# Optimization experiments

Hardware: AMD Instinct MI355X
Metric: run time of the kernel (lower is better)

Reference implementation:

```python
import jax, jax.numpy as jnp
import numpy as np

TOP_K = 2
LB_WEIGHT = 0.01


def _ln(x, g, b, eps=1e-5):
    m = x.mean(-1, keepdims=True)
    v = ((x - m) ** 2).mean(-1, keepdims=True)
    return (x - m) * jax.lax.rsqrt(v + eps) * g + b


def setup_inputs() -> dict:
    key = jax.random.key(0)
    ks = iter(jax.random.split(key, 40))
    B, L, D, CT, CB, E, H = 8, 1024, 1024, 768, 64, 8, 1024
    ID = 3 * D           # concat(id, content_proj, collab_proj)
    GH = max(ID // 2, 128)  # 1536, router gate hidden

    def rn(shape, s=0.02):
        return jax.random.normal(next(ks), shape, jnp.float32) * s

    return {
        "id_emb": rn((B, L, D), 1.0),
        "content_emb": rn((B, L, CT), 1.0),
        "collab_emb": rn((B, L, CB), 1.0),
        "ln_ct_g": jnp.ones(CT), "ln_ct_b": jnp.zeros(CT),
        "ln_cb_g": jnp.ones(CB), "ln_cb_b": jnp.zeros(CB),
        "Wc": rn((CT, D)), "bc": jnp.zeros(D),
        "Wcb": rn((CB, D)), "bcb": jnp.zeros(D),
        "Wg1": rn((ID, GH)), "bg1": jnp.zeros(GH),
        "lng_g": jnp.ones(GH), "lng_b": jnp.zeros(GH),
        "Wg2": rn((GH, GH // 2)), "bg2": jnp.zeros(GH // 2),
        "Wg3": rn((GH // 2, E)), "bg3": jnp.zeros(E),
        "We1": rn((E, ID, H)), "be1": jnp.zeros((E, H)),
        "lne1_g": jnp.ones((E, H)), "lne1_b": jnp.zeros((E, H)),
        "We2": rn((E, H, H // 2)), "be2": jnp.zeros((E, H // 2)),
        "We3": rn((E, H // 2, H // 4)), "be3": jnp.zeros((E, H // 4)),
        "lne3_g": jnp.ones((E, H // 4)), "lne3_b": jnp.zeros((E, H // 4)),
        "Wout": rn((H // 4, D)), "bout": jnp.zeros(D),
        "alpha": jnp.full((1,), 0.1, jnp.float32),
    }


def reference(id_emb, content_emb, collab_emb, ln_ct_g, ln_ct_b, ln_cb_g, ln_cb_b,
              Wc, bc, Wcb, bcb, Wg1, bg1, lng_g, lng_b, Wg2, bg2, Wg3, bg3,
              We1, be1, lne1_g, lne1_b, We2, be2, We3, be3, lne3_g, lne3_b,
              Wout, bout, alpha):
    # --- input normalization + projection to d_model (eval mode: no noise/dropout) ---
    ct = _ln(content_emb, ln_ct_g, ln_ct_b) @ Wc + bc        # (B,L,D)
    cb = _ln(collab_emb, ln_cb_g, ln_cb_b) @ Wcb + bcb       # (B,L,D)
    x = jnp.concatenate([id_emb, ct, cb], axis=-1)           # (B,L,3D)

    # --- router: gate MLP -> softmax -> top-k -> renormalize ---
    g = jax.nn.relu(_ln(x @ Wg1 + bg1, lng_g, lng_b))
    g = jax.nn.relu(g @ Wg2 + bg2)
    probs = jax.nn.softmax(g @ Wg3 + bg3, axis=-1)           # (B,L,E)
    topv, topi = jax.lax.top_k(probs, TOP_K)                 # (B,L,K)
    w = topv / (topv.sum(-1, keepdims=True) + 1e-8)

    # --- experts (dense over E, then gather selected) ---
    h = jax.nn.relu(_ln(jnp.einsum('bld,edh->bleh', x, We1) + be1, lne1_g, lne1_b))
    h = jax.nn.relu(jnp.einsum('bleh,ehm->blem', h, We2) + be2)
    eo = _ln(jnp.einsum('blem,emo->bleo', h, We3) + be3, lne3_g, lne3_b)  # (B,L,E,H/4)
    sel = jnp.take_along_axis(eo, topi[..., None], axis=2)   # (B,L,K,H/4)
    comb = (sel * w[..., None]).sum(axis=2)                  # (B,L,H/4)

    # --- output projection + learnable-alpha residual ---
    fused = id_emb + alpha * (comb @ Wout + bout)            # (B,L,D)

    # --- load balancing loss (importance + entropy terms) ---
    E = probs.shape[-1]
    num_tokens = probs.shape[0] * probs.shape[1]
    counts = jnp.sum(jax.nn.one_hot(topi, E, dtype=jnp.float32), axis=(0, 1, 2))
    f = counts / num_tokens
    P = probs.mean(axis=(0, 1))
    importance = E * (f * P).sum()
    ent = -(P * jnp.log(P + 1e-8)).sum()
    max_ent = jnp.log(jnp.asarray(E, jnp.float32))
    lb_loss = (importance + (max_ent - ent) / max_ent) * LB_WEIGHT
    return fused, lb_loss
```

## Files before the change

### kernel.cpp

```cpp
#include <hip/hip_runtime.h>
#include <hip/hip_bf16.h>

using u16 = unsigned short;
typedef float f32x4 __attribute__((ext_vector_type(4)));
typedef short short8 __attribute__((ext_vector_type(8)));
typedef unsigned short ushort8 __attribute__((ext_vector_type(8)));

typedef __attribute__((address_space(1))) const unsigned int gu32;
typedef __attribute__((address_space(3))) unsigned int lu32;

__device__ __forceinline__ float b2f(u16 u) {
  unsigned v = ((unsigned)u) << 16;
  float f;
  __builtin_memcpy(&f, &v, 4);
  return f;
}
__device__ __forceinline__ u16 f2b(float f) {
  unsigned u;
  __builtin_memcpy(&u, &f, 4);
  unsigned r = (u + 0x7fffu + ((u >> 16) & 1u)) >> 16;
  return (u16)r;
}
__device__ __forceinline__ float ldv(float x) { return x; }
__device__ __forceinline__ float ldv(u16 x) { return b2f(x); }

__device__ __forceinline__ void gl_lds16(const void* g, void* l) {
  __builtin_amdgcn_global_load_lds((gu32*)g, (lu32*)l, 16, 0, 0);
}

template <int D, bool RELU, bool PEREXP, typename TIN>
__global__ void ln_rows(const TIN* __restrict__ in, u16* __restrict__ out,
                        const float* __restrict__ gamma, const float* __restrict__ beta,
                        const int* __restrict__ pairExp, const int* __restrict__ total) {
  constexpr int T = (D >= 256) ? 256 : 64;
  constexpr int VPT = D / T;
  int row = blockIdx.x;
  if constexpr (PEREXP) {
    if (row >= *total) return;
  }
  int t = threadIdx.x;
  const TIN* r = in + (size_t)row * D;
  float vals[VPT];
  float s = 0.f, ss = 0.f;
#pragma unroll
  for (int i = 0; i < VPT; ++i) {
    float v = ldv(r[t + i * T]);
    vals[i] = v;
    s += v;
    ss += v * v;
  }
#pragma unroll
  for (int m = 1; m < 64; m <<= 1) {
    s += __shfl_xor(s, m);
    ss += __shfl_xor(ss, m);
  }
  if constexpr (T == 256) {
    __shared__ float red[8];
    int wave = t >> 6, lane = t & 63;
    if (lane == 0) { red[wave] = s; red[4 + wave] = ss; }
    __syncthreads();
    s = red[0] + red[1] + red[2] + red[3];
    ss = red[4] + red[5] + red[6] + red[7];
  }
  float mean = s / (float)D;
  float var = ss / (float)D - mean * mean;
  var = fmaxf(var, 0.f);
  float rstd = 1.f / sqrtf(var + 1e-5f);
  const float* g = gamma;
  const float* b = beta;
  if constexpr (PEREXP) {
    int e = pairExp[row];
    g += (size_t)e * D;
    b += (size_t)e * D;
  }
  u16* o = out + (size_t)row * D;
#pragma unroll
  for (int i = 0; i < VPT; ++i) {
    int idx = t + i * T;
    float v = (vals[i] - mean) * rstd * g[idx] + b[idx];
    if constexpr (RELU) v = fmaxf(v, 0.f);
    o[idx] = f2b(v);
  }
}

__global__ void prepackT(const float* __restrict__ in, u16* __restrict__ out,
                         int K, int M) {
  __shared__ u16 tile[64 * 65];
  size_t zo = (size_t)blockIdx.z * K * M;
  const float* ip = in + zo;
  u16* op = out + zo;
  int m0 = blockIdx.x * 64, k0 = blockIdx.y * 64;
  int t = threadIdx.x;
#pragma unroll
  for (int h = 0; h < 4; ++h) {
    int u = t + h * 256;
    int kr = u >> 4, mc = (u & 15) * 4;
    f32x4 v = *(const f32x4*)(ip + (size_t)(k0 + kr) * M + m0 + mc);
#pragma unroll
    for (int i = 0; i < 4; ++i) tile[kr * 65 + mc + i] = f2b(v[i]);
  }
  __syncthreads();
#pragma unroll
  for (int h = 0; h < 2; ++h) {
    int u = t + h * 256;
    int mr = u >> 3, kc = (u & 7) * 8;
    ushort8 v;
#pragma unroll
    for (int i = 0; i < 8; ++i) v[i] = tile[(kc + i) * 65 + mr];
    *(ushort8*)(op + (size_t)(m0 + mr) * K + k0 + kc) = v;
  }
}

__global__ void copy_id3(const float* __restrict__ id, u16* __restrict__ xb3) {
  size_t i = ((size_t)blockIdx.x * 256 + threadIdx.x) * 8;
  size_t t = i >> 10, d = i & 1023;
  f32x4 a = *(const f32x4*)(id + i);
  f32x4 b = *(const f32x4*)(id + i + 4);
  ushort8 v;
#pragma unroll
  for (int j = 0; j < 4; ++j) { v[j] = f2b(a[j]); v[j + 4] = f2b(b[j]); }
  *(ushort8*)(xb3 + t * 3072 + d) = v;
}

#define BM 128
#define BN 128
#define BK 32

template <int EPI, bool EXPERT, bool GATHER>
__global__ __launch_bounds__(256, 4)
void gemm_bf(const u16* __restrict__ A, const u16* __restrict__ Bt,
             const float* __restrict__ bias,
             u16* __restrict__ C, float* __restrict__ Cf,
             int K, int lda, int ldc,
             long strideB, int strideBias,
             const int* __restrict__ offA, const int* __restrict__ pairTok,
             const float* __restrict__ resid, const float* __restrict__ alphaPtr) {
  int rowTile = blockIdx.x * BM;
  int colTile = blockIdx.y * BN;
  if constexpr (EXPERT) {
    if (rowTile >= offA[8]) return;
    int e = 0;
    while (rowTile >= offA[e + 1]) ++e;
    Bt += (size_t)e * strideB;
    bias += (size_t)e * strideBias;
  }

  __shared__ u16 As[2][BM * BK];
  __shared__ u16 Bs[2][BN * BK];

  int t = threadIdx.x;
  int lane = t & 63;
  int wv = t >> 6;
  int wr = wv >> 1, wc = wv & 1;
  int l15 = lane & 15, l4 = lane >> 4;

  int c0 = wv, c1 = wv + 4;
  int r0 = c0 * 16 + (lane >> 2), r1 = c1 * 16 + (lane >> 2);
  int ac = (lane & 3) * 8;
  size_t aRow0, aRow1;
  if constexpr (GATHER) {
    aRow0 = (size_t)pairTok[rowTile + r0] * lda;
    aRow1 = (size_t)pairTok[rowTile + r1] * lda;
  } else {
    aRow0 = (size_t)(rowTile + r0) * lda;
    aRow1 = (size_t)(rowTile + r1) * lda;
  }
  const u16* aSrc0 = A + aRow0 + ac;
  const u16* aSrc1 = A + aRow1 + ac;
  const u16* bSrc0 = Bt + (size_t)(colTile + r0) * K + ac;
  const u16* bSrc1 = Bt + (size_t)(colTile + r1) * K + ac;

  auto STAGE = [&](int k0, int b) {
    gl_lds16(aSrc0 + k0, &As[b][c0 * 512]);
    gl_lds16(aSrc1 + k0, &As[b][c1 * 512]);
    gl_lds16(bSrc0 + k0, &Bs[b][c0 * 512]);
    gl_lds16(bSrc1 + k0, &Bs[b][c1 * 512]);
  };

  f32x4 zero4 = {0.f, 0.f, 0.f, 0.f};
  f32x4 acc[4][4];
#pragma unroll
  for (int m = 0; m < 4; ++m)
#pragma unroll
    for (int n = 0; n < 4; ++n) acc[m][n] = zero4;

  STAGE(0, 0);
  asm volatile("s_waitcnt vmcnt(0)" ::: "memory");
  __syncthreads();

  int nt = K / BK;
  for (int tt = 0; tt < nt; ++tt) {
    int cur = tt & 1;
    if (tt + 1 < nt) STAGE((tt + 1) * BK, cur ^ 1);
    short8 af[4], bf[4];
#pragma unroll
    for (int m = 0; m < 4; ++m)
      af[m] = *(const short8*)&As[cur][(wr * 64 + m * 16 + l15) * BK + l4 * 8];
#pragma unroll
    for (int n = 0; n < 4; ++n)
      bf[n] = *(const short8*)&Bs[cur][(wc * 64 + n * 16 + l15) * BK + l4 * 8];
#pragma unroll
    for (int m = 0; m < 4; ++m)
#pragma unroll
      for (int n = 0; n < 4; ++n)
        acc[m][n] = __builtin_amdgcn_mfma_f32_16x16x32_bf16(af[m], bf[n], acc[m][n], 0, 0, 0);
    asm volatile("s_waitcnt vmcnt(0)" ::: "memory");
    __syncthreads();
  }

  float alphaV = 0.f;
  if constexpr (EPI == 2) alphaV = alphaPtr[0];
#pragma unroll
  for (int n = 0; n < 4; ++n) {
    int col = colTile + wc * 64 + n * 16 + l15;
    float bv = bias[col];
#pragma unroll
    for (int m = 0; m < 4; ++m) {
      int r2 = rowTile + wr * 64 + m * 16 + l4 * 4;
#pragma unroll
      for (int j = 0; j < 4; ++j) {
        float v = acc[m][n][j] + bv;
        if constexpr (EPI == 1) v = fmaxf(v, 0.f);
        if constexpr (EPI == 2) {
          Cf[(size_t)(r2 + j) * ldc + col] =
              resid[(size_t)(r2 + j) * ldc + col] + alphaV * v;
        } else {
          C[(size_t)(r2 + j) * ldc + col] = f2b(v);
        }
      }
    }
  }
}

__global__ void router_kernel(const u16* __restrict__ g2, const float* __restrict__ Wg3,
                              const float* __restrict__ bg3, float* __restrict__ probs,
                              int* __restrict__ topi, float* __restrict__ wts) {
  int tok = blockIdx.x * 4 + (threadIdx.x >> 6);
  int lane = threadIdx.x & 63;
  const u16* row = g2 + (size_t)tok * 768;
  float acc[8];
#pragma unroll
  for (int e = 0; e < 8; ++e) acc[e] = 0.f;
  for (int j = lane; j < 768; j += 64) {
    float v = b2f(row[j]);
    f32x4 w0 = *(const f32x4*)(Wg3 + (size_t)j * 8);
    f32x4 w1 = *(const f32x4*)(Wg3 + (size_t)j * 8 + 4);
#pragma unroll
    for (int e = 0; e < 4; ++e) { acc[e] += v * w0[e]; acc[e + 4] += v * w1[e]; }
  }
#pragma unroll
  for (int e = 0; e < 8; ++e) {
#pragma unroll
    for (int m = 1; m < 64; m <<= 1) acc[e] += __shfl_xor(acc[e], m);
  }
  if (lane == 0) {
    float lg[8], mx = -3.4e38f;
#pragma unroll
    for (int e = 0; e < 8; ++e) {
      lg[e] = acc[e] + bg3[e];
      mx = fmaxf(mx, lg[e]);
    }
    float p[8], s = 0.f;
#pragma unroll
    for (int e = 0; e < 8; ++e) {
      p[e] = expf(lg[e] - mx);
      s += p[e];
    }
    float inv = 1.f / s;
#pragma unroll
    for (int e = 0; e < 8; ++e) {
      p[e] *= inv;
      probs[(size_t)tok * 8 + e] = p[e];
    }
    int i0 = 0;
    for (int e = 1; e < 8; ++e)
      if (p[e] > p[i0]) i0 = e;
    int i1 = (i0 == 0) ? 1 : 0;
    for (int e = 0; e < 8; ++e)
      if (e != i0 && p[e] > p[i1]) i1 = e;
    float w0 = p[i0], w1 = p[i1];
    float wsum = w0 + w1 + 1e-8f;
    topi[tok * 2] = i0;
    topi[tok * 2 + 1] = i1;
    wts[tok * 2] = w0 / wsum;
    wts[tok * 2 + 1] = w1 / wsum;
  }
}

__global__ void count_kernel(const int* __restrict__ topi, int* __restrict__ cnt,
                             int* __restrict__ offA, int* __restrict__ cursor) {
  __shared__ int c[8];
  int t = threadIdx.x;
  if (t < 8) c[t] = 0;
  __syncthreads();
  for (int i = t; i < 16384; i += 256) atomicAdd(&c[topi[i]], 1);
  __syncthreads();
  if (t == 0) {
    int off = 0;
    for (int e = 0; e < 8; ++e) {
      cnt[e] = c[e];
      offA[e] = off;
      cursor[e] = off;
      off += (c[e] + 127) & ~127;
    }
    offA[8] = off;
  }
}

__global__ void scatter_kernel(const int* __restrict__ topi, int* __restrict__ cursor,
                               int* __restrict__ pairTok, int* __restrict__ pairExp,
                               int* __restrict__ posOf) {
  int i = blockIdx.x * 256 + threadIdx.x;
  int e = topi[i];
  int pos = atomicAdd(&cursor[e], 1);
  pairTok[pos] = i >> 1;
  pairExp[pos] = e;
  posOf[i] = pos;
}

__global__ void padfill_kernel(const int* __restrict__ cnt, const int* __restrict__ offA,
                               int* __restrict__ pairTok, int* __restrict__ pairExp) {
  int e = blockIdx.x;
  int start = offA[e] + cnt[e];
  int end = offA[e + 1];
  for (int i = start + threadIdx.x; i < end; i += 256) {
    pairTok[i] = 0;
    pairExp[i] = e;
  }
}

__global__ void combine_kernel(const u16* __restrict__ eo, const int* __restrict__ posOf,
                               const float* __restrict__ wts, u16* __restrict__ comb) {
  int t = blockIdx.x, d = threadIdx.x;
  int p0 = posOf[t * 2], p1 = posOf[t * 2 + 1];
  float w0 = wts[t * 2], w1 = wts[t * 2 + 1];
  float v = w0 * b2f(eo[(size_t)p0 * 256 + d]) + w1 * b2f(eo[(size_t)p1 * 256 + d]);
  comb[(size_t)t * 256 + d] = f2b(v);
}

__global__ void lbloss_kernel(const float* __restrict__ probs, const int* __restrict__ cnt,
                              float* __restrict__ outp) {
  __shared__ float red[256];
  int t = threadIdx.x;
  float pl[8];
#pragma unroll
  for (int e = 0; e < 8; ++e) pl[e] = 0.f;
  for (int i = t; i < 8192; i += 256) {
#pragma unroll
    for (int e = 0; e < 8; ++e) pl[e] += probs[(size_t)i * 8 + e];
  }
  float P[8];
  for (int e = 0; e < 8; ++e) {
    red[t] = pl[e];
    __syncthreads();
    for (int s = 128; s > 0; s >>= 1) {
      if (t < s) red[t] += red[t + s];
      __syncthreads();
    }
    P[e] = red[0] / 8192.f;
    __syncthreads();
  }
  if (t == 0) {
    float imp = 0.f, ent = 0.f;
    for (int e = 0; e < 8; ++e) {
      float f = (float)cnt[e] / 8192.f;
      imp += f * P[e];
      ent -= P[e] * logf(P[e] + 1e-8f);
    }
    imp *= 8.f;
    float maxent = logf(8.f);
    outp[0] = (imp + (maxent - ent) / maxent) * 0.01f;
  }
}

extern "C" void kernel_launch(void* const* d_in, const int* in_sizes, int n_in,
                              void* d_out, int out_size, void* d_ws, size_t ws_size,
                              hipStream_t stream) {
  const float* id_emb   = (const float*)d_in[0];
  const float* content  = (const float*)d_in[1];
  const float* collab   = (const float*)d_in[2];
  const float* ln_ct_g  = (const float*)d_in[3];
  const float* ln_ct_b  = (const float*)d_in[4];
  const float* ln_cb_g  = (const float*)d_in[5];
  const float* ln_cb_b  = (const float*)d_in[6];
  const float* Wc       = (const float*)d_in[7];
  const float* bc       = (const float*)d_in[8];
  const float* Wcb      = (const float*)d_in[9];
  const float* bcb      = (const float*)d_in[10];
  const float* Wg1      = (const float*)d_in[11];
  const float* bg1      = (const float*)d_in[12];
  const float* lng_g    = (const float*)d_in[13];
  const float* lng_b    = (const float*)d_in[14];
  const float* Wg2      = (const float*)d_in[15];
  const float* bg2      = (const float*)d_in[16];
  const float* Wg3      = (const float*)d_in[17];
  const float* bg3      = (const float*)d_in[18];
  const float* We1      = (const float*)d_in[19];
  const float* be1      = (const float*)d_in[20];
  const float* lne1_g   = (const float*)d_in[21];
  const float* lne1_b   = (const float*)d_in[22];
  const float* We2      = (const float*)d_in[23];
  const float* be2      = (const float*)d_in[24];
  const float* We3      = (const float*)d_in[25];
  const float* be3      = (const float*)d_in[26];
  const float* lne3_g   = (const float*)d_in[27];
  const float* lne3_b   = (const float*)d_in[28];
  const float* Wout     = (const float*)d_in[29];
  const float* bout     = (const float*)d_in[30];
  const float* alpha    = (const float*)d_in[31];
  (void)in_sizes; (void)n_in; (void)out_size; (void)ws_size;

  float* out = (float*)d_out;
  char* ws = (char*)d_ws;
  size_t o = 0;
  auto AL = [&](size_t bytes) {
    size_t r = o;
    o += (bytes + 255) & ~(size_t)255;
    return r;
  };

  u16* WcT   = (u16*)(ws + AL(1024ull * 768 * 2));
  u16* WcbT  = (u16*)(ws + AL(1024ull * 64 * 2));
  u16* Wg1T  = (u16*)(ws + AL(1536ull * 3072 * 2));
  u16* Wg2T  = (u16*)(ws + AL(768ull * 1536 * 2));
  u16* We1T  = (u16*)(ws + AL(8ull * 1024 * 3072 * 2));
  u16* We2T  = (u16*)(ws + AL(8ull * 512 * 1024 * 2));
  u16* We3T  = (u16*)(ws + AL(8ull * 256 * 512 * 2));
  u16* WoutT = (u16*)(ws + AL(1024ull * 256 * 2));
  u16* xb3   = (u16*)(ws + AL(8192ull * 3072 * 2));
  size_t R1  = AL(17408ull * 1024 * 2);
  u16* ct_norm = (u16*)(ws + R1);
  u16* cb_norm = (u16*)(ws + R1 + 8192ull * 768 * 2);
  u16* g1      = (u16*)(ws + R1);
  u16* h1      = (u16*)(ws + R1);
  size_t R2  = AL(17408ull * 512 * 2);
  u16* g2 = (u16*)(ws + R2);
  u16* h2 = (u16*)(ws + R2);
  u16* eo   = (u16*)(ws + AL(17408ull * 256 * 2));
  u16* comb = (u16*)(ws + AL(8192ull * 256 * 2));
  float* probs = (float*)(ws + AL(8192ull * 8 * 4));
  int* topi    = (int*)(ws + AL(8192ull * 2 * 4));
  float* wts   = (float*)(ws + AL(8192ull * 2 * 4));
  int* posOf   = (int*)(ws + AL(8192ull * 2 * 4));
  int* pairTok = (int*)(ws + AL(17408ull * 4));
  int* pairExp = (int*)(ws + AL(17408ull * 4));
  int* cnt     = (int*)(ws + AL(64));
  int* offA    = (int*)(ws + AL(64));
  int* cursor  = (int*)(ws + AL(64));

  prepackT<<<dim3(16, 12), 256, 0, stream>>>(Wc, WcT, 768, 1024);
  prepackT<<<dim3(16, 1), 256, 0, stream>>>(Wcb, WcbT, 64, 1024);
  prepackT<<<dim3(24, 48), 256, 0, stream>>>(Wg1, Wg1T, 3072, 1536);
  prepackT<<<dim3(12, 24), 256, 0, stream>>>(Wg2, Wg2T, 1536, 768);
  prepackT<<<dim3(16, 48, 8), 256, 0, stream>>>(We1, We1T, 3072, 1024);
  prepackT<<<dim3(8, 16, 8), 256, 0, stream>>>(We2, We2T, 1024, 512);
  prepackT<<<dim3(4, 8, 8), 256, 0, stream>>>(We3, We3T, 512, 256);
  prepackT<<<dim3(16, 4), 256, 0, stream>>>(Wout, WoutT, 256, 1024);

  ln_rows<768, false, false, float><<<8192, 256, 0, stream>>>(content, ct_norm, ln_ct_g, ln_ct_b, nullptr, nullptr);
  ln_rows<64, false, false, float><<<8192, 64, 0, stream>>>(collab, cb_norm, ln_cb_g, ln_cb_b, nullptr, nullptr);
  copy_id3<<<4096, 256, 0, stream>>>(id_emb, xb3);
  gemm_bf<0, false, false><<<dim3(64, 8), 256, 0, stream>>>(
      ct_norm, WcT, bc, xb3 + 1024, nullptr, 768, 768, 3072,
      0, 0, nullptr, nullptr, nullptr, nullptr);
  gemm_bf<0, false, false><<<dim3(64, 8), 256, 0, stream>>>(
      cb_norm, WcbT, bcb, xb3 + 2048, nullptr, 64, 64, 3072,
      0, 0, nullptr, nullptr, nullptr, nullptr);

  gemm_bf<0, false, false><<<dim3(64, 12), 256, 0, stream>>>(
      xb3, Wg1T, bg1, g1, nullptr, 3072, 3072, 1536,
      0, 0, nullptr, nullptr, nullptr, nullptr);
  ln_rows<1536, true, false, u16><<<8192, 256, 0, stream>>>(g1, g1, lng_g, lng_b, nullptr, nullptr);
  gemm_bf<1, false, false><<<dim3(64, 6), 256, 0, stream>>>(
      g1, Wg2T, bg2, g2, nullptr, 1536, 1536, 768,
      0, 0, nullptr, nullptr, nullptr, nullptr);
  router_kernel<<<2048, 256, 0, stream>>>(g2, Wg3, bg3, probs, topi, wts);

  count_kernel<<<1, 256, 0, stream>>>(topi, cnt, offA, cursor);
  scatter_kernel<<<64, 256, 0, stream>>>(topi, cursor, pairTok, pairExp, posOf);
  padfill_kernel<<<8, 256, 0, stream>>>(cnt, offA, pairTok, pairExp);

  gemm_bf<0, true, true><<<dim3(136, 8), 256, 0, stream>>>(
      xb3, We1T, be1, h1, nullptr, 3072, 3072, 1024,
      3072l * 1024, 1024, offA, pairTok, nullptr, nullptr);
  ln_rows<1024, true, true, u16><<<17408, 256, 0, stream>>>(h1, h1, lne1_g, lne1_b, pairExp, offA + 8);
  gemm_bf<1, true, false><<<dim3(136, 4), 256, 0, stream>>>(
      h1, We2T, be2, h2, nullptr, 1024, 1024, 512,
      512l * 1024, 512, offA, nullptr, nullptr, nullptr);
  gemm_bf<0, true, false><<<dim3(136, 2), 256, 0, stream>>>(
      h2, We3T, be3, eo, nullptr, 512, 512, 256,
      256l * 512, 256, offA, nullptr, nullptr, nullptr);
  ln_rows<256, false, true, u16><<<17408, 256, 0, stream>>>(eo, eo, lne3_g, lne3_b, pairExp, offA + 8);
  combine_kernel<<<8192, 256, 0, stream>>>(eo, posOf, wts, comb);

  gemm_bf<2, false, false><<<dim3(64, 8), 256, 0, stream>>>(
      comb, WoutT, bout, nullptr, out, 256, 256, 1024,
      0, 0, nullptr, nullptr, id_emb, alpha);

  lbloss_kernel<<<1, 256, 0, stream>>>(probs, cnt, out + 8388608);
}
```

Before: 676.9 us.

## Widen GEMM tile to 128x256 and prefetch two stages ahead

The shared bf16 GEMM moves from 128x128 to 128x256 output tiles. Each wave now owns a 128x64 strip with 32 accumulators, and every launch grid halves its column-block count to match. The K loop is restructured so the next two stages are issued before the loop, with a partial vmcnt wait that overlaps loads with MFMA work instead of draining all loads each iteration. The aim is more operand reuse per LDS read and better load/compute overlap, at the cost of more registers, lower occupancy (launch bounds lowered from 4 to 2), and fewer blocks for the small GEMMs.

```diff
diff --git a/kernel.cpp b/kernel.cpp
--- a/kernel.cpp
+++ b/kernel.cpp
@@ -123,11 +123,11 @@
 }
 
 #define BM 128
-#define BN 128
+#define BN 256
 #define BK 32
 
 template <int EPI, bool EXPERT, bool GATHER>
-__global__ __launch_bounds__(256, 4)
+__global__ __launch_bounds__(256, 2)
 void gemm_bf(const u16* __restrict__ A, const u16* __restrict__ Bt,
              const float* __restrict__ bias,
              u16* __restrict__ C, float* __restrict__ Cf,
@@ -151,72 +151,77 @@
   int t = threadIdx.x;
   int lane = t & 63;
   int wv = t >> 6;
-  int wr = wv >> 1, wc = wv & 1;
   int l15 = lane & 15, l4 = lane >> 4;
 
-  int c0 = wv, c1 = wv + 4;
-  int r0 = c0 * 16 + (lane >> 2), r1 = c1 * 16 + (lane >> 2);
-  int ac = (lane & 3) * 8;
+  int rIn = lane >> 2, cIn = (lane & 3) * 8;
+  int ca0 = wv, ca1 = wv + 4;
   size_t aRow0, aRow1;
   if constexpr (GATHER) {
-    aRow0 = (size_t)pairTok[rowTile + r0] * lda;
-    aRow1 = (size_t)pairTok[rowTile + r1] * lda;
+    aRow0 = (size_t)pairTok[rowTile + ca0 * 16 + rIn] * lda;
+    aRow1 = (size_t)pairTok[rowTile + ca1 * 16 + rIn] * lda;
   } else {
-    aRow0 = (size_t)(rowTile + r0) * lda;
-    aRow1 = (size_t)(rowTile + r1) * lda;
-  }
-  const u16* aSrc0 = A + aRow0 + ac;
-  const u16* aSrc1 = A + aRow1 + ac;
-  const u16* bSrc0 = Bt + (size_t)(colTile + r0) * K + ac;
-  const u16* bSrc1 = Bt + (size_t)(colTile + r1) * K + ac;
+    aRow0 = (size_t)(rowTile + ca0 * 16 + rIn) * lda;
+    aRow1 = (size_t)(rowTile + ca1 * 16 + rIn) * lda;
+  }
+  const u16* aSrc0 = A + aRow0 + cIn;
+  const u16* aSrc1 = A + aRow1 + cIn;
+  const u16* bSrc[4];
+#pragma unroll
+  for (int i = 0; i < 4; ++i) {
+    int cb = 4 * wv + i;
+    bSrc[i] = Bt + (size_t)(colTile + cb * 16 + rIn) * K + cIn;
+  }
 
   auto STAGE = [&](int k0, int b) {
-    gl_lds16(aSrc0 + k0, &As[b][c0 * 512]);
-    gl_lds16(aSrc1 + k0, &As[b][c1 * 512]);
-    gl_lds16(bSrc0 + k0, &Bs[b][c0 * 512]);
-    gl_lds16(bSrc1 + k0, &Bs[b][c1 * 512]);
+    gl_lds16(aSrc0 + k0, &As[b][ca0 * 512]);
+    gl_lds16(aSrc1 + k0, &As[b][ca1 * 512]);
+#pragma unroll
+    for (int i = 0; i < 4; ++i) gl_lds16(bSrc[i] + k0, &Bs[b][(4 * wv + i) * 512]);
   };
 
   f32x4 zero4 = {0.f, 0.f, 0.f, 0.f};
-  f32x4 acc[4][4];
-#pragma unroll
-  for (int m = 0; m < 4; ++m)
+  f32x4 acc[8][4];
+#pragma unroll
+  for (int m = 0; m < 8; ++m)
 #pragma unroll
     for (int n = 0; n < 4; ++n) acc[m][n] = zero4;
 
+  int nt = K / BK;
   STAGE(0, 0);
-  asm volatile("s_waitcnt vmcnt(0)" ::: "memory");
-  __syncthreads();
-
-  int nt = K / BK;
+  if (nt > 1) STAGE(BK, 1);
+
   for (int tt = 0; tt < nt; ++tt) {
+    if (nt - tt >= 2)
+      asm volatile("s_waitcnt vmcnt(6)" ::: "memory");
+    else
+      asm volatile("s_waitcnt vmcnt(0)" ::: "memory");
+    __syncthreads();
     int cur = tt & 1;
-    if (tt + 1 < nt) STAGE((tt + 1) * BK, cur ^ 1);
-    short8 af[4], bf[4];
-#pragma unroll
-    for (int m = 0; m < 4; ++m)
-      af[m] = *(const short8*)&As[cur][(wr * 64 + m * 16 + l15) * BK + l4 * 8];
+    short8 af[8], bf[4];
+#pragma unroll
+    for (int m = 0; m < 8; ++m)
+      af[m] = *(const short8*)&As[cur][(m * 16 + l15) * BK + l4 * 8];
 #pragma unroll
     for (int n = 0; n < 4; ++n)
-      bf[n] = *(const short8*)&Bs[cur][(wc * 64 + n * 16 + l15) * BK + l4 * 8];
-#pragma unroll
-    for (int m = 0; m < 4; ++m)
+      bf[n] = *(const short8*)&Bs[cur][(wv * 64 + n * 16 + l15) * BK + l4 * 8];
+#pragma unroll
+    for (int m = 0; m < 8; ++m)
 #pragma unroll
       for (int n = 0; n < 4; ++n)
         acc[m][n] = __builtin_amdgcn_mfma_f32_16x16x32_bf16(af[m], bf[n], acc[m][n], 0, 0, 0);
-    asm volatile("s_waitcnt vmcnt(0)" ::: "memory");
     __syncthreads();
+    if (tt + 2 < nt) STAGE((tt + 2) * BK, cur);
   }
 
   float alphaV = 0.f;
   if constexpr (EPI == 2) alphaV = alphaPtr[0];
 #pragma unroll
   for (int n = 0; n < 4; ++n) {
-    int col = colTile + wc * 64 + n * 16 + l15;
+    int col = colTile + wv * 64 + n * 16 + l15;
     float bv = bias[col];
 #pragma unroll
-    for (int m = 0; m < 4; ++m) {
-      int r2 = rowTile + wr * 64 + m * 16 + l4 * 4;
+    for (int m = 0; m < 8; ++m) {
+      int r2 = rowTile + m * 16 + l4 * 4;
 #pragma unroll
       for (int j = 0; j < 4; ++j) {
         float v = acc[m][n][j] + bv;
@@ -460,18 +465,18 @@
   ln_rows<768, false, false, float><<<8192, 256, 0, stream>>>(content, ct_norm, ln_ct_g, ln_ct_b, nullptr, nullptr);
   ln_rows<64, false, false, float><<<8192, 64, 0, stream>>>(collab, cb_norm, ln_cb_g, ln_cb_b, nullptr, nullptr);
   copy_id3<<<4096, 256, 0, stream>>>(id_emb, xb3);
-  gemm_bf<0, false, false><<<dim3(64, 8), 256, 0, stream>>>(
+  gemm_bf<0, false, false><<<dim3(64, 4), 256, 0, stream>>>(
       ct_norm, WcT, bc, xb3 + 1024, nullptr, 768, 768, 3072,
       0, 0, nullptr, nullptr, nullptr, nullptr);
-  gemm_bf<0, false, false><<<dim3(64, 8), 256, 0, stream>>>(
+  gemm_bf<0, false, false><<<dim3(64, 4), 256, 0, stream>>>(
       cb_norm, WcbT, bcb, xb3 + 2048, nullptr, 64, 64, 3072,
       0, 0, nullptr, nullptr, nullptr, nullptr);
 
-  gemm_bf<0, false, false><<<dim3(64, 12), 256, 0, stream>>>(
+  gemm_bf<0, false, false><<<dim3(64, 6), 256, 0, stream>>>(
       xb3, Wg1T, bg1, g1, nullptr, 3072, 3072, 1536,
       0, 0, nullptr, nullptr, nullptr, nullptr);
   ln_rows<1536, true, false, u16><<<8192, 256, 0, stream>>>(g1, g1, lng_g, lng_b, nullptr, nullptr);
-  gemm_bf<1, false, false><<<dim3(64, 6), 256, 0, stream>>>(
+  gemm_bf<1, false, false><<<dim3(64, 3), 256, 0, stream>>>(
       g1, Wg2T, bg2, g2, nullptr, 1536, 1536, 768,
       0, 0, nullptr, nullptr, nullptr, nullptr);
   router_kernel<<<2048, 256, 0, stream>>>(g2, Wg3, bg3, probs, topi, wts);
@@ -480,20 +485,20 @@
   scatter_kernel<<<64, 256, 0, stream>>>(topi, cursor, pairTok, pairExp, posOf);
   padfill_kernel<<<8, 256, 0, stream>>>(cnt, offA, pairTok, pairExp);
 
-  gemm_bf<0, true, true><<<dim3(136, 8), 256, 0, stream>>>(
+  gemm_bf<0, true, true><<<dim3(136, 4), 256, 0, stream>>>(
       xb3, We1T, be1, h1, nullptr, 3072, 3072, 1024,
       3072l * 1024, 1024, offA, pairTok, nullptr, nullptr);
   ln_rows<1024, true, true, u16><<<17408, 256, 0, stream>>>(h1, h1, lne1_g, lne1_b, pairExp, offA + 8);
-  gemm_bf<1, true, false><<<dim3(136, 4), 256, 0, stream>>>(
+  gemm_bf<1, true, false><<<dim3(136, 2), 256, 0, stream>>>(
       h1, We2T, be2, h2, nullptr, 1024, 1024, 512,
       512l * 1024, 512, offA, nullptr, nullptr, nullptr);
-  gemm_bf<0, true, false><<<dim3(136, 2), 256, 0, stream>>>(
+  gemm_bf<0, true, false><<<dim3(136, 1), 256, 0, stream>>>(
       h2, We3T, be3, eo, nullptr, 512, 512, 256,
       256l * 512, 256, offA, nullptr, nullptr, nullptr);
   ln_rows<256, false, true, u16><<<17408, 256, 0, stream>>>(eo, eo, lne3_g, lne3_b, pairExp, offA + 8);
   combine_kernel<<<8192, 256, 0, stream>>>(eo, posOf, wts, comb);
 
-  gemm_bf<2, false, false><<<dim3(64, 8), 256, 0, stream>>>(
+  gemm_bf<2, false, false><<<dim3(64, 4), 256, 0, stream>>>(
       comb, WoutT, bout, nullptr, out, 256, 256, 1024,
       0, 0, nullptr, nullptr, id_emb, alpha);
 
```

New measurement: 745.9 us. 1.1x slower.
